# Kernel tuning notes

Hardware: AMD Instinct MI355X
Metric: run time of the kernel (lower is better)

The kernel has to match this reference:

```python
import jax, jax.numpy as jnp
import numpy as np

CAL = {
 'x': (-0.0025095, 0.0022181),
 'onnxMatMul_166': (-0.22075387835502625, 0.208940327167511),
 'fc1MatMul': (-0.00291599917, 0.0017367251),
 'fc1bias': (-0.48688140511512756, 0.5176185369491577),
 'fc1Add': (-0.48778465390205383, 0.5181604027748108),
 'Wiz_1': (-0.43284985423088074, 0.46175122261047363),
 'Wir_1': (-0.34401071071624756, 0.29191476106643677),
 'Win_1': (-0.3236880302429199, 0.39607325196266174),
 'Whz_1': (-1.8417714834213257, 1.7173254489898682),
 'Whr_1': (-1.1574513912200928, 1.0300449132919312),
 'Whn_1': (-0.7756922245025635, 0.9530389308929443),
 'biz_1': (-0.5063393712043762, 0.36664387583732605),
 'bir_1': (-0.07920225709676743, 0.20611026883125305),
 'bin_1': (-0.5539973378181458, 0.17938342690467834),
 'bhz_1': (-0.5337516665458679, 0.4148772358894348),
 'bhr_1': (-0.07688436657190323, 0.14814253151416779),
 'bhn_1': (-0.7828555107116699, 0.9008108973503113),
 'Wiz_2': (-0.9102030992507935, 0.9408696889877319),
 'Wir_2': (-0.9560997486114502, 0.6683358550071716),
 'Win_2': (-0.4721935987472534, 0.48561596870422363),
 'Whz_2': (-1.2992678880691528, 1.2991048097610474),
 'Whr_2': (-0.8318714499473572, 1.1085889339447021),
 'Whn_2': (-0.955470085144043, 1.046797513961792),
 'biz_2': (-0.44805487990379333, 0.1560053527355194),
 'bir_2': (-0.08767592161893845, 0.11347303539514542),
 'bin_2': (-0.239909827709198, 0.12033259868621826),
 'bhz_2': (-0.43745461106300354, 0.12699371576309204),
 'bhr_2': (-0.09617264568805695, 0.07690174877643585),
 'bhn_2': (-0.17204178869724274, 0.19739042222499847),
 'onnxMatMul_207': (-1.3657219409942627, 1.158295750617981),
 'fc2bias': (-0.1750922054052353, 0.1385071724653244),
 'onnxMatMul_208': (-3.1666038036346436, 2.5026357173919678),
 'fc3bias': (-0.10188056528568268, 0.0899151861667633),
 'onnxMatMul_209': (-1.300571084022522, 1.928941249847412),
 'fc4bias': (-0.10699586570262909, 0.04597663879394531),
 'h1': (-0.002647488145157695, 0.0028339680284261703),
 'h2': (-0.0031016061548143625, 0.0030250486452132463),
 'gru1_a_': (-0.6389939785003662, 0.7715625762939453),
 'gru1_a': (-0.6046768426895142, 0.8871182203292847),
 'gru1_b_': (-0.004922409541904926, 0.004103424027562141),
 'gru1_b': (-0.07475128024816513, 0.14630259573459625),
 'gru1_c_': (-1.5660111904144287, 1.0454494953155518),
 'gru1_c': (-1.9779117107391357, 1.3700535297393799),
 'gru1_d_': (-0.008429044857621193, 0.006403823848813772),
 'gru1_d': (-0.5529640316963196, 0.41507571935653687),
 'gru1_e_': (-1.3637111186981201, 1.018247127532959),
 'gru1_e': (-1.8583884239196777, 1.1587692499160767),
 'gru1_f_': (-0.005411399528384209, 0.0061536869034171104),
 'gru1_f': (-0.7833794355392456, 0.8978855013847351),
 'gru1_r_': (-0.6226556301116943, 0.9800534844398499),
 'gru1_r': (0.3491777181625366, 0.7271188497543335),
 'gru1_z_': (-2.392332077026367, 1.7851293087005615),
 'gru1_z': (0.08375928550958633, 0.856329083442688),
 'gru1_n1': (-0.5516456365585327, 0.4556601643562317),
 'gru1_n2': (-2.4100341796875, 1.1423156261444092),
 'gru1_n': (-0.983996570110321, 0.8151924014091492),
 'gru1_hn1': (0.143670916557312, 0.9162406921386719),
 'gru1_hn2': (-0.9015777111053467, 0.45391541719436646),
 'gru1_hn3': (-0.0016954239690676332, 0.0016671211924403906),
 'rnn1GRU': (-0.9016271829605103, 0.4546271562576294),
 'gru2_a_': (-0.681461751461029, 0.9113116264343262),
 'gru2_a': (-0.7149235010147095, 0.908741295337677),
 'gru2_b_': (-0.005148397758603096, 0.011014967225492),
 'gru2_b': (-0.09436552226543427, 0.07623167335987091),
 'gru2_c_': (-1.2279887199401855, 1.1102137565612793),
 'gru2_c': (-1.6760436296463013, 1.200895071029663),
 'gru2_d_': (-0.008141756057739258, 0.00894666276872158),
 'gru2_d': (-0.43875735998153687, 0.1262134611606598),
 'gru2_e_': (-0.6732944250106812, 0.6314664483070374),
}
# calib entries for gru2 past 'e_' were truncated in the source; reuse gru1 ranges
for _k in ['e', 'f_', 'f', 'r_', 'r', 'z_', 'z', 'n1', 'n2', 'n', 'hn1', 'hn2', 'hn3']:
    CAL.setdefault('gru2_' + _k, CAL['gru1_' + _k])
CAL['rnn2GRU'] = CAL['rnn1GRU']


def fq(x, name):
    """Per-tensor unsigned 8-bit fake-quantize/dequantize (CalibrationParam S/Z)."""
    mn, mx = CAL[name]
    s = (mx - mn) / 255.0  # 2**8 - 1
    z = float(round(-mn / s))
    q = jnp.clip(jnp.round(x / s) + z, 0.0, 255.0)
    y = (q - z) * s
    # straight-through: forward value is exact fake-quant, identity gradient
    return x + jax.lax.stop_gradient(y - x)


def _gru_layer(xs, Wiz, Wir, Win, Whz, Whr, Whn, biz, bir, binn, bhz, bhr, bhn, L):
    p = 'gru%d' % L
    Wiz = fq(Wiz, 'Wiz_%d' % L); Wir = fq(Wir, 'Wir_%d' % L); Win = fq(Win, 'Win_%d' % L)
    Whz = fq(Whz, 'Whz_%d' % L); Whr = fq(Whr, 'Whr_%d' % L); Whn = fq(Whn, 'Whn_%d' % L)
    biz = fq(biz, 'biz_%d' % L); bir = fq(bir, 'bir_%d' % L); binn = fq(binn, 'bin_%d' % L)
    bhz = fq(bhz, 'bhz_%d' % L); bhr = fq(bhr, 'bhr_%d' % L); bhn = fq(bhn, 'bhn_%d' % L)
    # input projections batched over all timesteps (xs: [T,B,H] time-major)
    A = fq(fq(jnp.einsum('tbi,ih->tbh', xs, Wir), p + '_a_') + bir, p + '_a')
    C = fq(fq(jnp.einsum('tbi,ih->tbh', xs, Wiz), p + '_c_') + biz, p + '_c')
    E = fq(fq(jnp.einsum('tbi,ih->tbh', xs, Win), p + '_e_') + binn, p + '_e')
    h0 = fq(jnp.zeros((xs.shape[1], Whz.shape[0]), xs.dtype), 'h%d' % L)

    def step(h, ace):
        a, c, e = ace
        b = fq(fq(h @ Whr, p + '_b_') + bhr, p + '_b')
        r = fq(jax.nn.sigmoid(fq(a + b, p + '_r_')), p + '_r')
        d = fq(fq(h @ Whz, p + '_d_') + bhz, p + '_d')
        z = fq(jax.nn.sigmoid(fq(c + d, p + '_z_')), p + '_z')
        f = fq(fq(h @ Whn, p + '_f_') + bhn, p + '_f')
        n = fq(jnp.tanh(fq(e + fq(r * f, p + '_n1'), p + '_n2')), p + '_n')
        hn2 = fq(fq(1.0 - z, p + '_hn1') * n, p + '_hn2')
        hn3 = fq(z * h, p + '_hn3')
        h_new = fq(hn2 + hn3, 'rnn%dGRU' % L)
        return h_new, h_new

    _, hs = jax.lax.scan(step, h0, (A, C, E))
    return hs


def setup_inputs() -> dict:
    B, T, F, H, D = 64, 1000, 257, 400, 600
    ks = iter(jax.random.split(jax.random.key(0), 64))

    def u(shape, name):
        mn, mx = CAL[name]
        return jax.random.uniform(next(ks), shape, jnp.float32, mn, mx)

    inp = {}
    inp['x'] = jax.random.normal(next(ks), (B, T, F), jnp.float32) * 0.001
    inp['W_fc1'] = u((F, H), 'onnxMatMul_166')
    inp['b_fc1'] = u((H,), 'fc1bias')
    for L in (1, 2):
        for g in ('z', 'r', 'n'):
            inp['Wi%s%d' % (g, L)] = u((H, H), 'Wi%s_%d' % (g, L))
            inp['Wh%s%d' % (g, L)] = u((H, H), 'Wh%s_%d' % (g, L))
            inp['bi%s%d' % (g, L)] = u((H,), 'bi%s_%d' % (g, L))
            inp['bh%s%d' % (g, L)] = u((H,), 'bh%s_%d' % (g, L))
    inp['W_fc2'] = u((H, D), 'onnxMatMul_207'); inp['b_fc2'] = u((D,), 'fc2bias')
    inp['W_fc3'] = u((D, D), 'onnxMatMul_208'); inp['b_fc3'] = u((D,), 'fc3bias')
    inp['W_fc4'] = u((D, F), 'onnxMatMul_209'); inp['b_fc4'] = u((F,), 'fc4bias')
    return inp


def reference(x, W_fc1, b_fc1, Wiz1, Wir1, Win1, Whz1, Whr1, Whn1, biz1, bir1, bin1, bhz1, bhr1, bhn1, Wiz2, Wir2, Win2, Whz2, Whr2, Whn2, biz2, bir2, bin2, bhz2, bhr2, bhn2, W_fc2, b_fc2, W_fc3, b_fc3, W_fc4, b_fc4):
    xq = fq(x, 'x')
    t = fq(jnp.einsum('bti,ih->bth', xq, fq(W_fc1, 'onnxMatMul_166')), 'fc1MatMul')
    t = fq(t + fq(b_fc1, 'fc1bias'), 'fc1Add')
    xs = jnp.swapaxes(t, 0, 1)  # [T,B,400]
    h1 = _gru_layer(xs, Wiz1, Wir1, Win1, Whz1, Whr1, Whn1, biz1, bir1, bin1, bhz1, bhr1, bhn1, 1)
    h2 = _gru_layer(h1, Wiz2, Wir2, Win2, Whz2, Whr2, Whn2, biz2, bir2, bin2, bhz2, bhr2, bhn2, 2)
    y = jnp.swapaxes(h2, 0, 1)  # [B,T,400]
    y = jax.nn.relu(jnp.einsum('bth,hd->btd', y, fq(W_fc2, 'onnxMatMul_207')) + fq(b_fc2, 'fc2bias'))
    y = jax.nn.relu(jnp.einsum('btd,de->bte', y, fq(W_fc3, 'onnxMatMul_208')) + fq(b_fc3, 'fc3bias'))
    y = jax.nn.sigmoid(jnp.einsum('bte,ef->btf', y, fq(W_fc4, 'onnxMatMul_209')) + fq(b_fc4, 'fc4bias'))
    return y
```

## Files before the change

### kernel.cpp

```cpp
#include <hip/hip_runtime.h>
#include <math.h>

#define DEV static __device__ __forceinline__

typedef int v4i __attribute__((ext_vector_type(4)));
typedef float v4f __attribute__((ext_vector_type(4)));
typedef __bf16 bf16_t;
typedef __bf16 v8bf __attribute__((ext_vector_type(8)));

struct SZ { float s, z; };

constexpr double cfloor_(double v){ long long i=(long long)v; return ((double)i > v) ? (double)(i-1) : (double)i; }
constexpr double cround_(double v){
  double fl = cfloor_(v); double fr = v - fl;
  return (fr > 0.5) ? fl + 1.0 : (fr < 0.5 ? fl : ((((long long)fl) & 1LL) == 0 ? fl : fl + 1.0));
}
constexpr SZ mksz(double mn, double mx){
  double s = (mx - mn) / 255.0;
  double z = cround_(-mn / s);
  return SZ{ (float)s, (float)z };
}

constexpr SZ Zx     = mksz(-0.0025095, 0.0022181);
constexpr SZ ZW1    = mksz(-0.22075387835502625, 0.208940327167511);
// ... 108 lines not shown
    float q = rintf(jb.W[m][k * 400 + j] / jb.s[m]) + jb.z[m];
    q = fminf(fmaxf(q, 0.f), 255.f);
    dst[i] = (unsigned char)q;
  }
}
__global__ __launch_bounds__(256) void kcolsum(const unsigned char* __restrict__ WhC, int* __restrict__ cs){
  int i = blockIdx.x * 256 + threadIdx.x;
  if (i < 2400) {
    const unsigned char* p = WhC + (size_t)i * 400;
    int s = 0;
    for (int k = 0; k < 400; ++k) s += p[k];
    cs[i] = s;
  }
}
__global__ __launch_bounds__(256) void kwic6(W6 jb, signed char* __restrict__ WiT, int* __restrict__ cs){
  for (int idx = blockIdx.x * 256 + threadIdx.x; idx < 960000; idx += gridDim.x * 256) {
    int m = idx / 160000, r = idx - m * 160000;
    int k = r / 400, n = r - k * 400;
    float q = rintf(jb.W[m][r] / jb.s[m]) + jb.z[m];
    q = fminf(fmaxf(q, 0.f), 255.f);
    int qi = (int)q;
    WiT[(size_t)m * 185600 + (size_t)n * 464 + k] = (signed char)(qi ^ 0x80);
    atomicAdd(&cs[m * 400 + n], qi - 128);
  }
  for (int idx = blockIdx.x * 256 + threadIdx.x; idx < 153600; idx += gridDim.x * 256) {
    int m = idx / 25600, r = idx - m * 25600;
    int n = r / 64, p = r - n * 64;
    WiT[(size_t)m * 185600 + (size_t)n * 464 + 400 + p] = 0;
  }
}
__global__ __launch_bounds__(256) void kwic(const float* __restrict__ W, signed char* __restrict__ Bt,
                                            int* __restrict__ cs, float s, float z, int K, int N){
  int total1 = K * N, total2 = (464 - K) * N;
  for (int idx = blockIdx.x * 256 + threadIdx.x; idx < total1; idx += gridDim.x * 256) {
    int k = idx / N, n = idx - k * N;
    float q = rintf(W[idx] / s) + z;
    q = fminf(fmaxf(q, 0.f), 255.f);
    int qi = (int)q;
    Bt[(size_t)n * 464 + k] = (signed char)(qi ^ 0x80);
    atomicAdd(&cs[n], qi - 128);
  }
  for (int idx = blockIdx.x * 256 + threadIdx.x; idx < total2; idx += gridDim.x * 256) {
    int n = idx / (464 - K), k = K + (idx - n * (464 - K));
    Bt[(size_t)n * 464 + k] = 0;
  }
}
__global__ __launch_bounds__(256) void kwbf(const float* __restrict__ W, bf16_t* __restrict__ Bt,
                                            float s, float z, int K, int N){
  int total1 = K * N, total2 = (608 - K) * N;
  for (int idx = blockIdx.x * 256 + threadIdx.x; idx < total1; idx += gridDim.x * 256) {
    int k = idx / N, n = idx - k * N;
    float q = rintf(W[idx] / s) + z;
    q = fminf(fmaxf(q, 0.f), 255.f);
    Bt[(size_t)n * 608 + k] = (bf16_t)(q - z);
  }
  for (int idx = blockIdx.x * 256 + threadIdx.x; idx < total2; idx += gridDim.x * 256) {
    int n = idx / (608 - K), k = K + (idx - n * (608 - K));
    Bt[(size_t)n * 608 + k] = (bf16_t)0.f;
  }
}
__global__ __launch_bounds__(256) void kxq(const float* __restrict__ x, unsigned char* __restrict__ xcq,
                                           float s, float z){
  int idx = blockIdx.x * 256 + threadIdx.x;
  if (idx < 64000 * 464) {
    int row = idx / 464, c = idx - row * 464;
    unsigned char code = 128;
    if (c < 257) {
      int bb = row & 63, tt = row >> 6;
      float q = rintf(x[((size_t)bb * 1000 + tt) * 257 + c] / s) + z;
      q = fminf(fmaxf(q, 0.f), 255.f);
      code = (unsigned char)q;
    }
    xcq[idx] = code;
  }
}
__global__ __launch_bounds__(256) void krsum(const unsigned char* __restrict__ A, int* __restrict__ rs,
                                             int w4){
  int r = blockIdx.x * 256 + threadIdx.x;
  const unsigned* p = (const unsigned*)(A + (size_t)r * (w4 * 16));
  unsigned s = 0;
  for (int i = 0; i < w4 * 4; ++i) s = udot4_(p[i], 0x01010101u, s);
  rs[r] = (int)s - 128 * 4 * (w4 * 4);
}
__global__ __launch_bounds__(256) void kinit(unsigned long long* __restrict__ hp1,
                                             unsigned long long* __restrict__ hp2, unsigned code){
  int i = blockIdx.x * 256 + threadIdx.x;
  if (i < 6400) {
    unsigned long long w = (unsigned long long)(code * 0x01010101u);
    hp1[i] = w; hp2[i] = w;
  }
}

__global__ __launch_bounds__(256) void gemm_i8(
    const unsigned char* __restrict__ Au8, int strideA, int aw4,
    const int* __restrict__ rowsum,
    const signed char* __restrict__ Bt, const int* __restrict__ colsum,
    const float* __restrict__ bias,
    unsigned char* __restrict__ outU8, float* __restrict__ outF,
    int N, int nb, int outStride, int epMode,
    int czw, int cza, int cconst, float ss,
    float e1S, float e1Z, float e2S, float e2Z)
{
  __shared__ __align__(16) signed char Asl[64 * 464];
  __shared__ __align__(16) signed char Bsl[80 * 464];
  const int tid = threadIdx.x;
  const int bm = blockIdx.x / nb;
  const int bn = blockIdx.x - bm * nb;
  const int m0 = bm * 64;
  const int n0 = bn * 80;
  for (int i = tid; i < 80 * 29; i += 256) {
    int r = i / 29, c = i - r * 29;
    uint4 v;
    if (n0 + r < N) v = *(const uint4*)(Bt + (size_t)(n0 + r) * 464 + c * 16);
    else { v.x = 0u; v.y = 0u; v.z = 0u; v.w = 0u; }
    *(uint4*)(Bsl + (size_t)r * 464 + c * 16) = v;
  }
  for (int i = tid; i < 64 * 29; i += 256) {
    int r = i / 29, c = i - r * 29;
    uint4 v;
    if (c < aw4) {
      v = *(const uint4*)(Au8 + (size_t)(m0 + r) * strideA + c * 16);
      v.x ^= 0x80808080u; v.y ^= 0x80808080u; v.z ^= 0x80808080u; v.w ^= 0x80808080u;
    } else { v.x = 0u; v.y = 0u; v.z = 0u; v.w = 0u; }
    *(uint4*)(Asl + (size_t)r * 464 + c * 16) = v;
  }
  __syncthreads();
  const int wv = tid >> 6, ln = tid & 63;
  const int lr = ln & 15;
  const int lk = ln >> 4;
  v4i acc[5];
#pragma unroll
  for (int j = 0; j < 5; ++j) { acc[j][0] = 0; acc[j][1] = 0; acc[j][2] = 0; acc[j][3] = 0; }
#pragma unroll
  for (int kc = 0; kc < 7; ++kc) {
    int kb = kc * 64 + lk * 16;
    v4i a = *(const v4i*)(Asl + (size_t)(wv * 16 + lr) * 464 + kb);
#pragma unroll
    for (int j = 0; j < 5; ++j) {
      v4i b = *(const v4i*)(Bsl + (size_t)(j * 16 + lr) * 464 + kb);
      acc[j] = __builtin_amdgcn_mfma_i32_16x16x64_i8(a, b, acc[j], 0, 0, 0);
    }
  }
#pragma unroll
  for (int reg = 0; reg < 4; ++reg) {
    int row = m0 + wv * 16 + lk * 4 + reg;
    int RA = rowsum[row];
#pragma unroll
    for (int j = 0; j < 5; ++j) {
      int col = n0 + j * 16 + lr;
      if (col >= N) continue;
      int I = acc[j][reg] + czw * RA + cza * colsum[col] + cconst;
      float v = (float)I * ss;
      if (epMode == 0) {
        v = fq_(v, e1S, e1Z) + bias[col];
        float q = rintf(v / e2S) + e2Z;
        q = fminf(fmaxf(q, 0.f), 255.f);
        outU8[(size_t)row * outStride + col] = (unsigned char)q;
      } else {
        v += bias[col];
        v = fmaxf(v, 0.f);
        outF[(size_t)row * outStride + col] = v;
      }
    }
  }
}

__global__ __launch_bounds__(512) void gemm_bf(
    const float* __restrict__ A, const bf16_t* __restrict__ Bt,
    const float* __restrict__ bias, float* __restrict__ outF,
    int N, int nb, int epMode, int rowOff, float sc)
{
  __shared__ __align__(16) bf16_t Bs[128 * 616];
  const int tid = threadIdx.x;
  const int bm = blockIdx.x / nb;
  const int bn = blockIdx.x - bm * nb;
  const int m0 = bm * 128;
  const int n0 = bn * 128;
  for (int i = tid; i < 128 * 76; i += 512) {
    int r = i / 76, c = i - r * 76;
    uint4 v; v.x = 0u; v.y = 0u; v.z = 0u; v.w = 0u;
    if (n0 + r < N) v = *(const uint4*)((const char*)(Bt + (size_t)(n0 + r) * 608) + c * 16);
    *(uint4*)((char*)(Bs + (size_t)r * 616) + c * 16) = v;
  }
  __syncthreads();
  const int wv = tid >> 6, ln = tid & 63;
  const int lr = ln & 15, quad = ln >> 4;
  const float* arp = A + (size_t)(m0 + wv * 16 + lr) * 600;
  v4f acc[8];
#pragma unroll
  for (int j = 0; j < 8; ++j) { acc[j][0] = 0.f; acc[j][1] = 0.f; acc[j][2] = 0.f; acc[j][3] = 0.f; }
  for (int kc = 0; kc < 19; ++kc) {
    int kb = kc * 32 + quad * 8;
    float af[8];
    if (kc == 18 && quad == 3) {
#pragma unroll
      for (int j = 0; j < 8; ++j) af[j] = 0.f;
    } else {
      *(float4*)&af[0] = *(const float4*)(arp + kb);
      *(float4*)&af[4] = *(const float4*)(arp + kb + 4);
    }
    v8bf ah, al;
#pragma unroll
    for (int j = 0; j < 8; ++j) {
      float xx = af[j];
      bf16_t h = (bf16_t)xx;
      ah[j] = h;
      al[j] = (bf16_t)(xx - (float)h);
    }
#pragma unroll
    for (int nf = 0; nf < 8; ++nf) {
      v8bf bfrag = *(const v8bf*)(Bs + (size_t)(nf * 16 + lr) * 616 + kc * 32 + quad * 8);
      acc[nf] = __builtin_amdgcn_mfma_f32_16x16x32_bf16(ah, bfrag, acc[nf], 0, 0, 0);
      acc[nf] = __builtin_amdgcn_mfma_f32_16x16x32_bf16(al, bfrag, acc[nf], 0, 0, 0);
    }
  }
#pragma unroll
  for (int nf = 0; nf < 8; ++nf) {
    int col = n0 + nf * 16 + lr;
    if (col >= N) continue;
    float bcol = bias[col];
#pragma unroll
    for (int reg = 0; reg < 4; ++reg) {
      int row = m0 + wv * 16 + quad * 4 + reg;
      float v = acc[nf][reg] * sc + bcol;
      if (epMode == 2) {
        v = fmaxf(v, 0.f);
        outF[(size_t)row * N + col] = v;
      } else {
        v = sigm_(v);
        int rg = rowOff + row;
        int tt = rg >> 6, bb = rg & 63;
        outF[((size_t)bb * 1000 + tt) * 257 + col] = v;
      }
    }
  }
}

__global__ __launch_bounds__(384) void gru_rec(
    const unsigned char* __restrict__ WhC, const int* __restrict__ colsum,
    const unsigned char* __restrict__ Aq, const unsigned char* __restrict__ Cq,
    const unsigned char* __restrict__ Eq,
    const float* __restrict__ bhr, const float* __restrict__ bhz, const float* __restrict__ bhn,
    unsigned char* __restrict__ hs,
    unsigned long long* hpub, RecP P)
{
  __shared__ __align__(16) uint4 Wlds[9600];
  __shared__ __align__(16) uint4 hq_own[7];
  __shared__ __align__(16) uint4 hqr[21];
  __shared__ float dots[2][3][100];
  __shared__ unsigned aceb[75];
  __shared__ int HqS_s;
  __shared__ int flag;

  const int tid = threadIdx.x;
  const int wv  = tid >> 6;
  const int ln  = tid & 63;
  const int b   = blockIdx.x & 63;
  const int sl  = blockIdx.x >> 6;
  const int jbase = sl * 100;

  unsigned* Wled = (unsigned*)Wlds;
  unsigned* hqow = (unsigned*)hq_own;
  unsigned* hqrw = (unsigned*)hqr;

  for (int idx = tid; idx < 30000; idx += 384) {
    int cid0 = idx / 100, w = idx - cid0 * 100;
    int c = w / 25, p = w - c * 25;
    int g0 = cid0 / 100, jj0 = cid0 - g0 * 100;
    unsigned word = ((const unsigned*)(WhC + ((size_t)(g0 * 400) + jbase + jj0) * 400))[w];
    int slot = (c * 7 + (p >> 2)) ^ (cid0 & 31);
    Wled[cid0 * 128 + slot * 4 + (p & 3)] = word;
  }
  for (int idx = tid; idx < 3600; idx += 384) {
    int cid0 = idx / 12, r = idx - cid0 * 12;
    int c = r / 3, wd = r - c * 3 + 1;
    int slot = (c * 7 + 6) ^ (cid0 & 31);
    Wled[cid0 * 128 + slot * 4 + wd] = 0u;
  }
  const unsigned code0 = (unsigned)fminf(fmaxf(P.rnn.z, 0.f), 255.f);
  if (tid < 28) hqow[tid] = (tid < 25) ? code0 * 0x01010101u : 0u;
  if (tid >= 32 && tid < 41) {
    int r = tid - 32; int o = r / 3, wd = r - o * 3 + 1;
    hqrw[o * 28 + 24 + wd] = 0u;
  }
  if (tid == 383) flag = -1;

  const int cid = tid;
  int g = cid / 100;
  int jj = cid - g * 100;
  float s1S = 1.f, s1Z = 0.f, s2S = 1.f, s2Z = 0.f, biasj = 0.f, swsh = 0.f;
  int zwi = 0, CSj = 0;
  if (tid < 300) {
    int j = jbase + jj;
    SZ w  = (g == 0) ? P.wr : (g == 1) ? P.wz : P.wn;
    SZ s1 = (g == 0) ? P.b1 : (g == 1) ? P.d1 : P.f1;
    SZ s2 = (g == 0) ? P.b2 : (g == 1) ? P.d2 : P.f2;
    zwi = (int)w.z;
    s1S = s1.s; s1Z = s1.z; s2S = s2.s; s2Z = s2.z;
    biasj = ((g == 0) ? bhr : (g == 1) ? bhz : bhn)[j];
    CSj = colsum[g * 400 + j];
    swsh = w.s * P.rnn.s;
  }
  const int zhi = (int)P.rnn.z;
  const int swm = cid & 31;

  unsigned hprev = code0;
  __syncthreads();

  for (int t = 0; t < 1000; ++t) {
    if (wv == 5) {
      size_t row = (size_t)t * 64 + b;
      int w0 = ln, w1 = 64 + ln;
      int wh0 = w0 / 25, wi0 = w0 - wh0 * 25;
      const unsigned char* p0 = (wh0 == 0) ? Aq : (wh0 == 1) ? Cq : Eq;
      unsigned v0 = *(const unsigned*)(p0 + row * 400 + jbase + wi0 * 4);
      unsigned v1 = 0;
      if (ln < 11) {
        int wh1 = w1 / 25, wi1 = w1 - wh1 * 25;
        const unsigned char* p1 = (wh1 == 0) ? Aq : (wh1 == 1) ? Cq : Eq;
        v1 = *(const unsigned*)(p1 + row * 400 + jbase + wi1 * 4);
      }
      const unsigned long long* base = hpub + ((size_t)(t & 3) * 64 + b) * 100;
      unsigned pay0, pay1 = 0;
      {
        int o = ln / 25, p = ln - o * 25;
        int so = (sl + o + 1) & 3;
        const unsigned long long* src = base + so * 25 + p;
        unsigned long long w64;
        while ((unsigned)((w64 = __hip_atomic_load(src, __ATOMIC_RELAXED, __HIP_MEMORY_SCOPE_AGENT)) >> 32)
               != (unsigned)t) { }
        pay0 = (unsigned)w64;
        hqrw[o * 28 + ((p >> 2) * 4) + (p & 3)] = pay0;
      }
      if (ln < 11) {
        int widx = 64 + ln;
        int o = widx / 25, p = widx - o * 25;
        int so = (sl + o + 1) & 3;
        const unsigned long long* src = base + so * 25 + p;
        unsigned long long w64;
        while ((unsigned)((w64 = __hip_atomic_load(src, __ATOMIC_RELAXED, __HIP_MEMORY_SCOPE_AGENT)) >> 32)
               != (unsigned)t) { }
        pay1 = (unsigned)w64;
        hqrw[o * 28 + ((p >> 2) * 4) + (p & 3)] = pay1;
      }
      unsigned hp = udot4_(pay0, 0x01010101u, 0u);
      if (ln < 11) hp = udot4_(pay1, 0x01010101u, hp);
      if (ln < 25) hp = udot4_(hqow[ln], 0x01010101u, hp);
#pragma unroll
      for (int off = 32; off; off >>= 1) hp += __shfl_down(hp, off, 64);
      if (ln == 0) HqS_s = (int)hp;
      __hip_atomic_store(&flag, t, __ATOMIC_RELEASE, __HIP_MEMORY_SCOPE_WORKGROUP);
      aceb[ln] = v0;
      if (ln < 11) aceb[64 + ln] = v1;
      if (t > 0 && ln < 25)
        *(unsigned*)(hs + ((size_t)(t - 1) * 64 + b) * 400 + jbase + ln * 4) = hqow[ln];
    } else if (tid < 300) {
      unsigned acc = 0;
      const uint4* wcol = &Wlds[cid * 32];
#pragma unroll
      for (int i = 0; i < 7; ++i) {
        uint4 h = hq_own[i];
        uint4 w = wcol[(sl * 7 + i) ^ swm];
        acc = udot4_(w.x, h.x, acc);
        acc = udot4_(w.y, h.y, acc);
        acc = udot4_(w.z, h.z, acc);
        acc = udot4_(w.w, h.w, acc);
      }
      while (__hip_atomic_load(&flag, __ATOMIC_ACQUIRE, __HIP_MEMORY_SCOPE_WORKGROUP) < t)
        __builtin_amdgcn_s_sleep(1);
#pragma unroll
      for (int o = 0; o < 3; ++o) {
        int c = (sl + o + 1) & 3;
#pragma unroll
        for (int i = 0; i < 7; ++i) {
          uint4 h = hqr[o * 7 + i];
          uint4 w = wcol[(c * 7 + i) ^ swm];
          acc = udot4_(w.x, h.x, acc);
          acc = udot4_(w.y, h.y, acc);
          acc = udot4_(w.z, h.z, acc);
          acc = udot4_(w.w, h.w, acc);
        }
      }
      int I = (int)acc - zwi * HqS_s - zhi * CSj + 400 * zhi * zwi;
      float dot = (float)I * swsh;
      float v = fq_(dot, s1S, s1Z) + biasj;
      v = fq_(v, s2S, s2Z);
      dots[t & 1][g][jj] = v;
    }
    __syncthreads();
    if (tid < 128) {
      int m = (tid < 100) ? tid : 99;
      const unsigned char* aceb8 = (const unsigned char*)aceb;
      float a = ((float)aceb8[m]       - P.a.z) * P.a.s;
      float c = ((float)aceb8[100 + m] - P.c.z) * P.c.s;
      float e = ((float)aceb8[200 + m] - P.e.z) * P.e.s;
      float bb = dots[t & 1][0][m], dd = dots[t & 1][1][m], ff = dots[t & 1][2][m];
      float r  = fq_(sigm_(fq_(a + bb, P.r1.s, P.r1.z)), P.r2.s, P.r2.z);
      float zz = fq_(sigm_(fq_(c + dd, P.z1.s, P.z1.z)), P.z2.s, P.z2.z);
      float nn = fq_(tanhf(fq_(e + fq_(r * ff, P.n1.s, P.n1.z), P.n2.s, P.n2.z)), P.n3.s, P.n3.z);
      float hold = ((float)hprev - P.rnn.z) * P.rnn.s;
      float hn2v = fq_(fq_(1.f - zz, P.hn1.s, P.hn1.z) * nn, P.hn2.s, P.hn2.z);
      float hn3v = fq_(zz * hold, P.hn3.s, P.hn3.z);
      float hnew = hn2v + hn3v;
      float q = rintf(hnew / P.rnn.s) + P.rnn.z;
      q = fminf(fmaxf(q, 0.f), 255.f);
      unsigned code = (unsigned)q;
      unsigned c1 = __shfl_down(code, 1);
      unsigned c2 = __shfl_down(code, 2);
      unsigned c3 = __shfl_down(code, 3);
      if (tid < 100) {
        if ((tid & 3) == 0) {
          unsigned packed = code | (c1 << 8) | (c2 << 16) | (c3 << 24);
          unsigned long long out64 = ((unsigned long long)(unsigned)(t + 1) << 32) | packed;
          unsigned long long* dst = hpub + ((size_t)((t + 1) & 3) * 64 + b) * 100 + sl * 25 + (tid >> 2);
          __hip_atomic_store(dst, out64, __ATOMIC_RELAXED, __HIP_MEMORY_SCOPE_AGENT);
          hqow[tid >> 2] = packed;
        }
        hprev = code;
      }
    }
    __syncthreads();
  }
  if (wv == 5 && ln < 25)
    *(unsigned*)(hs + ((size_t)999 * 64 + b) * 400 + jbase + ln * 4) = hqow[ln];
}

extern "C" void kernel_launch(void* const* d_in, const int* in_sizes, int n_in,
                              void* d_out, int out_size, void* d_ws, size_t ws_size,
                              hipStream_t stream)
{
  const float* x    = (const float*)d_in[0];
  const float* Wfc1 = (const float*)d_in[1];
  const float* bfc1 = (const float*)d_in[2];
  const float* Wiz1 = (const float*)d_in[3];  const float* Whz1 = (const float*)d_in[4];
  const float* biz1 = (const float*)d_in[5];  const float* bhz1 = (const float*)d_in[6];
  const float* Wir1 = (const float*)d_in[7];  const float* Whr1 = (const float*)d_in[8];
  const float* bir1 = (const float*)d_in[9];  const float* bhr1 = (const float*)d_in[10];
  const float* Win1 = (const float*)d_in[11]; const float* Whn1 = (const float*)d_in[12];
  const float* bin1 = (const float*)d_in[13]; const float* bhn1 = (const float*)d_in[14];
  const float* Wiz2 = (const float*)d_in[15]; const float* Whz2 = (const float*)d_in[16];
  const float* biz2 = (const float*)d_in[17]; const float* bhz2 = (const float*)d_in[18];
  const float* Wir2 = (const float*)d_in[19]; const float* Whr2 = (const float*)d_in[20];
  const float* bir2 = (const float*)d_in[21]; const float* bhr2 = (const float*)d_in[22];
  const float* Win2 = (const float*)d_in[23]; const float* Whn2 = (const float*)d_in[24];
  const float* bin2 = (const float*)d_in[25]; const float* bhn2 = (const float*)d_in[26];
  const float* Wfc2 = (const float*)d_in[27]; const float* bfc2 = (const float*)d_in[28];
  const float* Wfc3 = (const float*)d_in[29]; const float* bfc3 = (const float*)d_in[30];
  const float* Wfc4 = (const float*)d_in[31]; const float* bfc4 = (const float*)d_in[32];
  float* out = (float*)d_out;

  char* wp = (char*)d_ws;
  auto alloc = [&](size_t bytes) -> void* {
    void* p = (void*)wp;
    wp += (bytes + 255) & ~(size_t)255;
    return p;
  };
  float* b1q = (float*)alloc(400 * 4);
  float* biq = (float*)alloc(2400 * 4);
  float* bhq = (float*)alloc(2400 * 4);
  float* b2q = (float*)alloc(600 * 4);
  float* b3q = (float*)alloc(600 * 4);
  float* b4q = (float*)alloc(257 * 4);
  unsigned char* WhC = (unsigned char*)alloc(960000);
  int* colsum = (int*)alloc(2400 * 4);
  signed char* WiT = (signed char*)alloc(7 * 400 * 464);
  signed char* Bt2 = (signed char*)alloc(600 * 464);
  bf16_t* Bt3 = (bf16_t*)alloc(600 * 608 * 2);
  bf16_t* Bt4 = (bf16_t*)alloc(257 * 608 * 2);
  int* cwi = (int*)alloc((7 * 400 + 600) * 4);
  int* rsX1 = (int*)alloc(64000 * 4);
  int* rsX  = (int*)alloc(64000 * 4);
  int* rsH  = (int*)alloc(64000 * 4);
  int* rsH2 = (int*)alloc(64000 * 4);
  unsigned char* xsq = (unsigned char*)alloc(25600000);
  unsigned char* Aq  = (unsigned char*)alloc(25600000);
  unsigned char* Cq  = (unsigned char*)alloc(25600000);
  unsigned char* Eq  = (unsigned char*)alloc(25600000);
  unsigned char* hs1 = (unsigned char*)alloc(25600000);
  unsigned char* hs2 = (unsigned char*)alloc(25600000);
  unsigned long long* hpub1 = (unsigned long long*)alloc(4 * 64 * 100 * 8);
  unsigned long long* hpub2 = (unsigned long long*)alloc(4 * 64 * 100 * 8);
  float* y2c = (float*)Aq;
  float* y3c = (float*)(Aq + 38400000);
  unsigned char* xcq = hs1;

  BJobs bj;
  bj.j[0]  = { bfc1, b1q,        400, Zbfc1.s, Zbfc1.z };
  bj.j[1]  = { bir1, biq + 0,    400, Zbir1.s, Zbir1.z };
  bj.j[2]  = { biz1, biq + 400,  400, Zbiz1.s, Zbiz1.z };
  bj.j[3]  = { bin1, biq + 800,  400, Zbin1.s, Zbin1.z };
  bj.j[4]  = { bir2, biq + 1200, 400, Zbir2.s, Zbir2.z };
  bj.j[5]  = { biz2, biq + 1600, 400, Zbiz2.s, Zbiz2.z };
  bj.j[6]  = { bin2, biq + 2000, 400, Zbin2.s, Zbin2.z };
  bj.j[7]  = { bhr1, bhq + 0,    400, Zbhr1.s, Zbhr1.z };
  bj.j[8]  = { bhz1, bhq + 400,  400, Zbhz1.s, Zbhz1.z };
  bj.j[9]  = { bhn1, bhq + 800,  400, Zbhn1.s, Zbhn1.z };
  bj.j[10] = { bhr2, bhq + 1200, 400, Zbhr2.s, Zbhr2.z };
  bj.j[11] = { bhz2, bhq + 1600, 400, Zbhz2.s, Zbhz2.z };
  bj.j[12] = { bhn2, bhq + 2000, 400, Zbhn2.s, Zbhn2.z };
  bj.j[13] = { bfc2, b2q,        600, Zbfc2.s, Zbfc2.z };
  bj.j[14] = { bfc3, b3q,        600, Zbfc3.s, Zbfc3.z };
  bj.j[15] = { bfc4, b4q,        257, Zbfc4.s, Zbfc4.z };
  kbias<<<dim3(16), dim3(256), 0, stream>>>(bj);

  W6 wh = { { Whr1, Whz1, Whn1, Whr2, Whz2, Whn2 },
            { ZWhr1.s, ZWhz1.s, ZWhn1.s, ZWhr2.s, ZWhz2.s, ZWhn2.s },
            { ZWhr1.z, ZWhz1.z, ZWhn1.z, ZWhr2.z, ZWhz2.z, ZWhn2.z } };
  kwhc6<<<dim3(3750), dim3(256), 0, stream>>>(wh, WhC);
  kcolsum<<<dim3(10), dim3(256), 0, stream>>>(WhC, colsum);
  unsigned code0 = (unsigned)(Zrnn.z < 0.f ? 0.f : (Zrnn.z > 255.f ? 255.f : Zrnn.z));
  kinit<<<dim3(25), dim3(256), 0, stream>>>(hpub1, hpub2, code0);

  hipMemsetAsync(cwi, 0, (7 * 400 + 600) * 4, stream);
  W6 wi = { { Wir1, Wiz1, Win1, Wir2, Wiz2, Win2 },
            { ZWir1.s, ZWiz1.s, ZWin1.s, ZWir2.s, ZWiz2.s, ZWin2.s },
            { ZWir1.z, ZWiz1.z, ZWin1.z, ZWir2.z, ZWiz2.z, ZWin2.z } };
  kwic6<<<dim3(625), dim3(256), 0, stream>>>(wi, WiT, cwi);
  kwic<<<dim3(625), dim3(256), 0, stream>>>(Wfc1, WiT + (size_t)6 * 185600, cwi + 2400, ZW1.s, ZW1.z, 257, 400);
  kwic<<<dim3(625), dim3(256), 0, stream>>>(Wfc2, Bt2, cwi + 2800, ZWfc2.s, ZWfc2.z, 400, 600);
  kwbf<<<dim3(625), dim3(256), 0, stream>>>(Wfc3, Bt3, ZWfc3.s, ZWfc3.z, 600, 600);
  kwbf<<<dim3(625), dim3(256), 0, stream>>>(Wfc4, Bt4, ZWfc4.s, ZWfc4.z, 600, 257);

  auto gi8 = [&](const unsigned char* A, int strideA, int aw4, const int* rs,
                 const signed char* Bt, const int* cs, const float* bias,
                 unsigned char* oU8, float* oF, int M, int N, int outStride, int epMode,
                 SZ a, SZ w, int Kreal, float ss, SZ e1, SZ e2) {
    int czw = 128 - (int)w.z, cza = 128 - (int)a.z;
    int cconst = Kreal * cza * czw;
    int nb = (N + 79) / 80;
    gemm_i8<<<dim3((M / 64) * nb), dim3(256), 0, stream>>>(
        A, strideA, aw4, rs, Bt, cs, bias, oU8, oF, N, nb, outStride, epMode,
        czw, cza, cconst, ss, e1.s, e1.z, e2.s, e2.z);
  };

  kxq<<<dim3((64000 * 464 + 255) / 256), dim3(256), 0, stream>>>(x, xcq, Zx.s, Zx.z);
  krsum<<<dim3(250), dim3(256), 0, stream>>>(xcq, rsX1, 29);
  gi8(xcq, 464, 29, rsX1, WiT + (size_t)6 * 185600, cwi + 2400, b1q,
      xsq, nullptr, 64000, 400, 400, 0, Zx, ZW1, 257, Zx.s * ZW1.s, Zfc1mm, Zfc1add);

  krsum<<<dim3(250), dim3(256), 0, stream>>>(xsq, rsX, 25);
  gi8(xsq, 400, 25, rsX, WiT + (size_t)0 * 185600, cwi + 0,    biq + 0,   Aq, nullptr,
      64000, 400, 400, 0, Zfc1add, ZWir1, 400, Zfc1add.s * ZWir1.s, Za_1, Za1);
  gi8(xsq, 400, 25, rsX, WiT + (size_t)1 * 185600, cwi + 400,  biq + 400, Cq, nullptr,
      64000, 400, 400, 0, Zfc1add, ZWiz1, 400, Zfc1add.s * ZWiz1.s, Zc_1, Zc1);
  gi8(xsq, 400, 25, rsX, WiT + (size_t)2 * 185600, cwi + 800,  biq + 800, Eq, nullptr,
      64000, 400, 400, 0, Zfc1add, ZWin1, 400, Zfc1add.s * ZWin1.s, Ze_1, Ze1);
  gru_rec<<<dim3(256), dim3(384), 0, stream>>>(WhC, colsum, Aq, Cq, Eq,
                                               bhq + 0, bhq + 400, bhq + 800,
                                               hs1, hpub1, PL1);
  krsum<<<dim3(250), dim3(256), 0, stream>>>(hs1, rsH, 25);
  gi8(hs1, 400, 25, rsH, WiT + (size_t)3 * 185600, cwi + 1200, biq + 1200, Aq, nullptr,
      64000, 400, 400, 0, Zrnn, ZWir2, 400, Zrnn.s * ZWir2.s, Za_2, Za2);
  gi8(hs1, 400, 25, rsH, WiT + (size_t)4 * 185600, cwi + 1600, biq + 1600, Cq, nullptr,
      64000, 400, 400, 0, Zrnn, ZWiz2, 400, Zrnn.s * ZWiz2.s, Zc_2, Zc2);
  gi8(hs1, 400, 25, rsH, WiT + (size_t)5 * 185600, cwi + 2000, biq + 2000, Eq, nullptr,
      64000, 400, 400, 0, Zrnn, ZWin2, 400, Zrnn.s * ZWin2.s, Ze_2, Ze1);
  gru_rec<<<dim3(256), dim3(384), 0, stream>>>(WhC + 480000, colsum + 1200, Aq, Cq, Eq,
                                               bhq + 1200, bhq + 1600, bhq + 2000,
                                               hs2, hpub2, PL2);
  krsum<<<dim3(250), dim3(256), 0, stream>>>(hs2, rsH2, 25);
  for (int rc = 0; rc < 4; ++rc) {
    const unsigned char* a2 = hs2 + (size_t)rc * 16000 * 400;
    gi8(a2, 400, 25, rsH2 + rc * 16000, Bt2, cwi + 2800, b2q, nullptr, y2c,
        16000, 600, 600, 2, Zrnn, ZWfc2, 400, Zrnn.s * ZWfc2.s, Zrnn, Zrnn);
    gemm_bf<<<dim3(125 * 5), dim3(512), 0, stream>>>(y2c, Bt3, b3q, y3c, 600, 5, 2, 0, ZWfc3.s);
    gemm_bf<<<dim3(125 * 3), dim3(512), 0, stream>>>(y3c, Bt4, b4q, out, 257, 3, 3, rc * 16000, ZWfc4.s);
  }
  (void)in_sizes; (void)n_in; (void)out_size; (void)ws_size;
}
```

Before: 7.347 ms.

## Run each GRU batch row in a single 768-thread block without cross-block flags

Measured after the change: 13.37 ms. 1.82x slower.

```diff
diff --git a/kernel.cpp b/kernel.cpp
--- a/kernel.cpp
+++ b/kernel.cpp
@@ -214,14 +214,6 @@
   for (int i = 0; i < w4 * 4; ++i) s = udot4_(p[i], 0x01010101u, s);
   rs[r] = (int)s - 128 * 4 * (w4 * 4);
 }
-__global__ __launch_bounds__(256) void kinit(unsigned long long* __restrict__ hp1,
-                                             unsigned long long* __restrict__ hp2, unsigned code){
-  int i = blockIdx.x * 256 + threadIdx.x;
-  if (i < 6400) {
-    unsigned long long w = (unsigned long long)(code * 0x01010101u);
-    hp1[i] = w; hp2[i] = w;
-  }
-}
 
 __global__ __launch_bounds__(256) void gemm_i8(
     const unsigned char* __restrict__ Au8, int strideA, int aw4,
@@ -368,193 +360,190 @@
   }
 }
 
-__global__ __launch_bounds__(384) void gru_rec(
+__global__ __launch_bounds__(768) void gru_rec64(
     const unsigned char* __restrict__ WhC, const int* __restrict__ colsum,
     const unsigned char* __restrict__ Aq, const unsigned char* __restrict__ Cq,
     const unsigned char* __restrict__ Eq,
     const float* __restrict__ bhr, const float* __restrict__ bhz, const float* __restrict__ bhn,
-    unsigned char* __restrict__ hs,
-    unsigned long long* hpub, RecP P)
+    unsigned char* __restrict__ hs, RecP P)
 {
-  __shared__ __align__(16) uint4 Wlds[9600];
-  __shared__ __align__(16) uint4 hq_own[7];
-  __shared__ __align__(16) uint4 hqr[21];
-  __shared__ float dots[2][3][100];
-  __shared__ unsigned aceb[75];
-  __shared__ int HqS_s;
-  __shared__ int flag;
+  __shared__ __align__(16) unsigned Wl[960 * 28];
+  __shared__ __align__(16) unsigned hq[2][4 * 28];
+  __shared__ int dots_i[1200];
+  __shared__ unsigned acew[2][300];
+  __shared__ int ic_l[1200];
+  __shared__ float bias_l[1200];
+  __shared__ int HqS[2];
 
   const int tid = threadIdx.x;
-  const int wv  = tid >> 6;
-  const int ln  = tid & 63;
-  const int b   = blockIdx.x & 63;
-  const int sl  = blockIdx.x >> 6;
-  const int jbase = sl * 100;
-
-  unsigned* Wled = (unsigned*)Wlds;
-  unsigned* hqow = (unsigned*)hq_own;
-  unsigned* hqrw = (unsigned*)hqr;
-
-  for (int idx = tid; idx < 30000; idx += 384) {
-    int cid0 = idx / 100, w = idx - cid0 * 100;
-    int c = w / 25, p = w - c * 25;
-    int g0 = cid0 / 100, jj0 = cid0 - g0 * 100;
-    unsigned word = ((const unsigned*)(WhC + ((size_t)(g0 * 400) + jbase + jj0) * 400))[w];
-    int slot = (c * 7 + (p >> 2)) ^ (cid0 & 31);
-    Wled[cid0 * 128 + slot * 4 + (p & 3)] = word;
-  }
-  for (int idx = tid; idx < 3600; idx += 384) {
-    int cid0 = idx / 12, r = idx - cid0 * 12;
-    int c = r / 3, wd = r - c * 3 + 1;
-    int slot = (c * 7 + 6) ^ (cid0 & 31);
-    Wled[cid0 * 128 + slot * 4 + wd] = 0u;
+  const int b = blockIdx.x;
+  const unsigned* Wu = (const unsigned*)WhC;
+
+  unsigned wq[5][25];
+#pragma unroll
+  for (int s = 0; s < 5; ++s) {
+    int q = tid + 768 * s;
+    const unsigned* src = Wu + (q >> 2) * 100 + (q & 3) * 25;
+#pragma unroll
+    for (int w = 0; w < 25; ++w) wq[s][w] = src[w];
+  }
+  for (int i = tid; i < 960 * 25; i += 768) {
+    int ql = i / 25, w = i - ql * 25;
+    int q = 3840 + ql;
+    Wl[ql * 28 + w] = Wu[(q >> 2) * 100 + (q & 3) * 25 + w];
+  }
+  const int zh = (int)P.rnn.z;
+  for (int d = tid; d < 1200; d += 768) {
+    int g = (d >= 800) ? 2 : (d >= 400 ? 1 : 0);
+    int zw = (g == 0) ? (int)P.wr.z : (g == 1) ? (int)P.wz.z : (int)P.wn.z;
+    ic_l[d] = -zh * colsum[d] + 400 * zh * zw;
+    int j = d - g * 400;
+    bias_l[d] = ((g == 0) ? bhr : (g == 1) ? bhz : bhn)[j];
   }
   const unsigned code0 = (unsigned)fminf(fmaxf(P.rnn.z, 0.f), 255.f);
-  if (tid < 28) hqow[tid] = (tid < 25) ? code0 * 0x01010101u : 0u;
-  if (tid >= 32 && tid < 41) {
-    int r = tid - 32; int o = r / 3, wd = r - o * 3 + 1;
-    hqrw[o * 28 + 24 + wd] = 0u;
-  }
-  if (tid == 383) flag = -1;
-
-  const int cid = tid;
-  int g = cid / 100;
-  int jj = cid - g * 100;
-  float s1S = 1.f, s1Z = 0.f, s2S = 1.f, s2Z = 0.f, biasj = 0.f, swsh = 0.f;
-  int zwi = 0, CSj = 0;
-  if (tid < 300) {
-    int j = jbase + jj;
-    SZ w  = (g == 0) ? P.wr : (g == 1) ? P.wz : P.wn;
-    SZ s1 = (g == 0) ? P.b1 : (g == 1) ? P.d1 : P.f1;
-    SZ s2 = (g == 0) ? P.b2 : (g == 1) ? P.d2 : P.f2;
-    zwi = (int)w.z;
-    s1S = s1.s; s1Z = s1.z; s2S = s2.s; s2Z = s2.z;
-    biasj = ((g == 0) ? bhr : (g == 1) ? bhz : bhn)[j];
-    CSj = colsum[g * 400 + j];
-    swsh = w.s * P.rnn.s;
-  }
-  const int zhi = (int)P.rnn.z;
-  const int swm = cid & 31;
-
-  unsigned hprev = code0;
+  for (int i = tid; i < 100; i += 768)
+    hq[0][(i / 25) * 28 + (i % 25)] = code0 * 0x01010101u;
+  if (tid == 0) { HqS[0] = 400 * (int)code0; HqS[1] = 0; }
+  const unsigned char* psrc = nullptr;
+  int poff = 0;
+  if (tid >= 400 && tid < 700) {
+    int idx = tid - 400;
+    int g = idx / 100, w = idx - g * 100;
+    psrc = (g == 0) ? Aq : (g == 1) ? Cq : Eq;
+    poff = w * 4;
+    acew[0][idx] = *(const unsigned*)(psrc + (size_t)b * 400 + poff);
+  }
   __syncthreads();
 
+  const int part = tid & 3;
+  const int grp = tid >> 2;
+  const unsigned* hbase0 = &hq[0][part * 28];
+  const unsigned* hbase1 = &hq[1][part * 28];
+  const unsigned* wl5 = &Wl[tid * 28];
+  const unsigned* wl6 = &Wl[(768 + (tid & 191)) * 28];
+  const int zwr = (int)P.wr.z, zwz = (int)P.wz.z, zwn = (int)P.wn.z;
+  const float swr = P.wr.s * P.rnn.s, swz = P.wz.s * P.rnn.s, swn = P.wn.s * P.rnn.s;
+
+  unsigned pf = 0;
+  unsigned hcode = code0;
+
   for (int t = 0; t < 1000; ++t) {
-    if (wv == 5) {
-      size_t row = (size_t)t * 64 + b;
-      int w0 = ln, w1 = 64 + ln;
-      int wh0 = w0 / 25, wi0 = w0 - wh0 * 25;
-      const unsigned char* p0 = (wh0 == 0) ? Aq : (wh0 == 1) ? Cq : Eq;
-      unsigned v0 = *(const unsigned*)(p0 + row * 400 + jbase + wi0 * 4);
-      unsigned v1 = 0;
-      if (ln < 11) {
-        int wh1 = w1 / 25, wi1 = w1 - wh1 * 25;
-        const unsigned char* p1 = (wh1 == 0) ? Aq : (wh1 == 1) ? Cq : Eq;
-        v1 = *(const unsigned*)(p1 + row * 400 + jbase + wi1 * 4);
+    if (tid >= 400 && tid < 700) {
+      int tn = (t + 1 < 1000) ? (t + 1) : 999;
+      pf = *(const unsigned*)(psrc + ((size_t)tn * 64 + b) * 400 + poff);
+    }
+    if (tid == 767) HqS[(t + 1) & 1] = 0;
+    const unsigned* hb = (t & 1) ? hbase1 : hbase0;
+    unsigned a0 = 0, a1 = 0, a2 = 0, a3 = 0, a4 = 0, a5 = 0, a6 = 0;
+#pragma unroll
+    for (int c = 0; c < 6; ++c) {
+      uint4 h4 = *(const uint4*)(hb + 4 * c);
+      uint4 w5 = *(const uint4*)(wl5 + 4 * c);
+      a0 = udot4_(wq[0][4*c+0], h4.x, a0);
+      a0 = udot4_(wq[0][4*c+1], h4.y, a0);
+      a0 = udot4_(wq[0][4*c+2], h4.z, a0);
+      a0 = udot4_(wq[0][4*c+3], h4.w, a0);
+      a1 = udot4_(wq[1][4*c+0], h4.x, a1);
+      a1 = udot4_(wq[1][4*c+1], h4.y, a1);
+      a1 = udot4_(wq[1][4*c+2], h4.z, a1);
+      a1 = udot4_(wq[1][4*c+3], h4.w, a1);
+      a2 = udot4_(wq[2][4*c+0], h4.x, a2);
+      a2 = udot4_(wq[2][4*c+1], h4.y, a2);
+      a2 = udot4_(wq[2][4*c+2], h4.z, a2);
+      a2 = udot4_(wq[2][4*c+3], h4.w, a2);
+      a3 = udot4_(wq[3][4*c+0], h4.x, a3);
+      a3 = udot4_(wq[3][4*c+1], h4.y, a3);
+      a3 = udot4_(wq[3][4*c+2], h4.z, a3);
+      a3 = udot4_(wq[3][4*c+3], h4.w, a3);
+      a4 = udot4_(wq[4][4*c+0], h4.x, a4);
+      a4 = udot4_(wq[4][4*c+1], h4.y, a4);
+      a4 = udot4_(wq[4][4*c+2], h4.z, a4);
+      a4 = udot4_(wq[4][4*c+3], h4.w, a4);
+      a5 = udot4_(w5.x, h4.x, a5);
+      a5 = udot4_(w5.y, h4.y, a5);
+      a5 = udot4_(w5.z, h4.z, a5);
+      a5 = udot4_(w5.w, h4.w, a5);
+      if (tid < 192) {
+        uint4 w6 = *(const uint4*)(wl6 + 4 * c);
+        a6 = udot4_(w6.x, h4.x, a6);
+        a6 = udot4_(w6.y, h4.y, a6);
+        a6 = udot4_(w6.z, h4.z, a6);
+        a6 = udot4_(w6.w, h4.w, a6);
       }
-      const unsigned long long* base = hpub + ((size_t)(t & 3) * 64 + b) * 100;
-      unsigned pay0, pay1 = 0;
-      {
-        int o = ln / 25, p = ln - o * 25;
-        int so = (sl + o + 1) & 3;
-        const unsigned long long* src = base + so * 25 + p;
-        unsigned long long w64;
-        while ((unsigned)((w64 = __hip_atomic_load(src, __ATOMIC_RELAXED, __HIP_MEMORY_SCOPE_AGENT)) >> 32)
-               != (unsigned)t) { }
-        pay0 = (unsigned)w64;
-        hqrw[o * 28 + ((p >> 2) * 4) + (p & 3)] = pay0;
-      }
-      if (ln < 11) {
-        int widx = 64 + ln;
-        int o = widx / 25, p = widx - o * 25;
-        int so = (sl + o + 1) & 3;
-        const unsigned long long* src = base + so * 25 + p;
-        unsigned long long w64;
-        while ((unsigned)((w64 = __hip_atomic_load(src, __ATOMIC_RELAXED, __HIP_MEMORY_SCOPE_AGENT)) >> 32)
-               != (unsigned)t) { }
-        pay1 = (unsigned)w64;
-        hqrw[o * 28 + ((p >> 2) * 4) + (p & 3)] = pay1;
-      }
-      unsigned hp = udot4_(pay0, 0x01010101u, 0u);
-      if (ln < 11) hp = udot4_(pay1, 0x01010101u, hp);
-      if (ln < 25) hp = udot4_(hqow[ln], 0x01010101u, hp);
-#pragma unroll
-      for (int off = 32; off; off >>= 1) hp += __shfl_down(hp, off, 64);
-      if (ln == 0) HqS_s = (int)hp;
-      __hip_atomic_store(&flag, t, __ATOMIC_RELEASE, __HIP_MEMORY_SCOPE_WORKGROUP);
-      aceb[ln] = v0;
-      if (ln < 11) aceb[64 + ln] = v1;
-      if (t > 0 && ln < 25)
-        *(unsigned*)(hs + ((size_t)(t - 1) * 64 + b) * 400 + jbase + ln * 4) = hqow[ln];
-    } else if (tid < 300) {
-      unsigned acc = 0;
-      const uint4* wcol = &Wlds[cid * 32];
-#pragma unroll
-      for (int i = 0; i < 7; ++i) {
-        uint4 h = hq_own[i];
-        uint4 w = wcol[(sl * 7 + i) ^ swm];
-        acc = udot4_(w.x, h.x, acc);
-        acc = udot4_(w.y, h.y, acc);
-        acc = udot4_(w.z, h.z, acc);
-        acc = udot4_(w.w, h.w, acc);
-      }
-      while (__hip_atomic_load(&flag, __ATOMIC_ACQUIRE, __HIP_MEMORY_SCOPE_WORKGROUP) < t)
-        __builtin_amdgcn_s_sleep(1);
-#pragma unroll
-      for (int o = 0; o < 3; ++o) {
-        int c = (sl + o + 1) & 3;
-#pragma unroll
-        for (int i = 0; i < 7; ++i) {
-          uint4 h = hqr[o * 7 + i];
-          uint4 w = wcol[(c * 7 + i) ^ swm];
-          acc = udot4_(w.x, h.x, acc);
-          acc = udot4_(w.y, h.y, acc);
-          acc = udot4_(w.z, h.z, acc);
-          acc = udot4_(w.w, h.w, acc);
-        }
-      }
-      int I = (int)acc - zwi * HqS_s - zhi * CSj + 400 * zhi * zwi;
-      float dot = (float)I * swsh;
-      float v = fq_(dot, s1S, s1Z) + biasj;
-      v = fq_(v, s2S, s2Z);
-      dots[t & 1][g][jj] = v;
+    }
+    {
+      unsigned hl = hb[24];
+      a0 = udot4_(wq[0][24], hl, a0);
+      a1 = udot4_(wq[1][24], hl, a1);
+      a2 = udot4_(wq[2][24], hl, a2);
+      a3 = udot4_(wq[3][24], hl, a3);
+      a4 = udot4_(wq[4][24], hl, a4);
+      a5 = udot4_(wl5[24], hl, a5);
+      if (tid < 192) a6 = udot4_(wl6[24], hl, a6);
+    }
+    a0 += __shfl_xor(a0, 1); a0 += __shfl_xor(a0, 2);
+    a1 += __shfl_xor(a1, 1); a1 += __shfl_xor(a1, 2);
+    a2 += __shfl_xor(a2, 1); a2 += __shfl_xor(a2, 2);
+    a3 += __shfl_xor(a3, 1); a3 += __shfl_xor(a3, 2);
+    a4 += __shfl_xor(a4, 1); a4 += __shfl_xor(a4, 2);
+    a5 += __shfl_xor(a5, 1); a5 += __shfl_xor(a5, 2);
+    a6 += __shfl_xor(a6, 1); a6 += __shfl_xor(a6, 2);
+    {
+      int v0 = (part == 0) ? (int)a0 : (part == 1) ? (int)a1 : (part == 2) ? (int)a2 : (int)a3;
+      dots_i[grp + 192 * part] = v0;
+      if (part == 0)      dots_i[grp + 768]  = (int)a4;
+      else if (part == 1) dots_i[grp + 960]  = (int)a5;
+      else if (part == 2) { if (grp < 48) dots_i[grp + 1152] = (int)a6; }
     }
     __syncthreads();
-    if (tid < 128) {
-      int m = (tid < 100) ? tid : 99;
-      const unsigned char* aceb8 = (const unsigned char*)aceb;
-      float a = ((float)aceb8[m]       - P.a.z) * P.a.s;
-      float c = ((float)aceb8[100 + m] - P.c.z) * P.c.s;
-      float e = ((float)aceb8[200 + m] - P.e.z) * P.e.s;
-      float bb = dots[t & 1][0][m], dd = dots[t & 1][1][m], ff = dots[t & 1][2][m];
-      float r  = fq_(sigm_(fq_(a + bb, P.r1.s, P.r1.z)), P.r2.s, P.r2.z);
-      float zz = fq_(sigm_(fq_(c + dd, P.z1.s, P.z1.z)), P.z2.s, P.z2.z);
-      float nn = fq_(tanhf(fq_(e + fq_(r * ff, P.n1.s, P.n1.z), P.n2.s, P.n2.z)), P.n3.s, P.n3.z);
-      float hold = ((float)hprev - P.rnn.z) * P.rnn.s;
+
+    unsigned ps = 0;
+    if (tid < 400) {
+      const int j = tid;
+      const unsigned char* ab = (const unsigned char*)&acew[t & 1][0];
+      float av = ((float)ab[j]       - P.a.z) * P.a.s;
+      float cv = ((float)ab[400 + j] - P.c.z) * P.c.s;
+      float ev = ((float)ab[800 + j] - P.e.z) * P.e.s;
+      int hqs = HqS[t & 1];
+      int Ib = dots_i[j]       - zwr * hqs + ic_l[j];
+      int Id = dots_i[400 + j] - zwz * hqs + ic_l[400 + j];
+      int If = dots_i[800 + j] - zwn * hqs + ic_l[800 + j];
+      float bb = fq_((float)Ib * swr, P.b1.s, P.b1.z) + bias_l[j];
+      bb = fq_(bb, P.b2.s, P.b2.z);
+      float dd = fq_((float)Id * swz, P.d1.s, P.d1.z) + bias_l[400 + j];
+      dd = fq_(dd, P.d2.s, P.d2.z);
+      float ff = fq_((float)If * swn, P.f1.s, P.f1.z) + bias_l[800 + j];
+      ff = fq_(ff, P.f2.s, P.f2.z);
+      float r  = fq_(sigm_(fq_(av + bb, P.r1.s, P.r1.z)), P.r2.s, P.r2.z);
+      float zz = fq_(sigm_(fq_(cv + dd, P.z1.s, P.z1.z)), P.z2.s, P.z2.z);
+      float nn = fq_(tanhf(fq_(ev + fq_(r * ff, P.n1.s, P.n1.z), P.n2.s, P.n2.z)), P.n3.s, P.n3.z);
+      float hold = ((float)hcode - P.rnn.z) * P.rnn.s;
       float hn2v = fq_(fq_(1.f - zz, P.hn1.s, P.hn1.z) * nn, P.hn2.s, P.hn2.z);
       float hn3v = fq_(zz * hold, P.hn3.s, P.hn3.z);
       float hnew = hn2v + hn3v;
-      float q = rintf(hnew / P.rnn.s) + P.rnn.z;
-      q = fminf(fmaxf(q, 0.f), 255.f);
-      unsigned code = (unsigned)q;
+      float qv = rintf(hnew / P.rnn.s) + P.rnn.z;
+      qv = fminf(fmaxf(qv, 0.f), 255.f);
+      unsigned code = (unsigned)qv;
+      hcode = code;
       unsigned c1 = __shfl_down(code, 1);
       unsigned c2 = __shfl_down(code, 2);
       unsigned c3 = __shfl_down(code, 3);
-      if (tid < 100) {
-        if ((tid & 3) == 0) {
-          unsigned packed = code | (c1 << 8) | (c2 << 16) | (c3 << 24);
-          unsigned long long out64 = ((unsigned long long)(unsigned)(t + 1) << 32) | packed;
-          unsigned long long* dst = hpub + ((size_t)((t + 1) & 3) * 64 + b) * 100 + sl * 25 + (tid >> 2);
-          __hip_atomic_store(dst, out64, __ATOMIC_RELAXED, __HIP_MEMORY_SCOPE_AGENT);
-          hqow[tid >> 2] = packed;
-        }
-        hprev = code;
+      if ((j & 3) == 0) {
+        unsigned packed = code | (c1 << 8) | (c2 << 16) | (c3 << 24);
+        int wrd = j >> 2;
+        int pp = wrd / 25, off = wrd - pp * 25;
+        hq[(t + 1) & 1][pp * 28 + off] = packed;
+        *(unsigned*)(hs + ((size_t)t * 64 + b) * 400 + (wrd << 2)) = packed;
+        ps = udot4_(packed, 0x01010101u, 0u);
       }
-    }
+    } else if (tid < 700) {
+      acew[(t + 1) & 1][tid - 400] = pf;
+    }
+#pragma unroll
+    for (int off = 32; off; off >>= 1) ps += __shfl_down(ps, off);
+    if ((tid & 63) == 0) atomicAdd(&HqS[(t + 1) & 1], (int)ps);
     __syncthreads();
   }
-  if (wv == 5 && ln < 25)
-    *(unsigned*)(hs + ((size_t)999 * 64 + b) * 400 + jbase + ln * 4) = hqow[ln];
 }
 
 extern "C" void kernel_launch(void* const* d_in, const int* in_sizes, int n_in,
@@ -610,8 +599,6 @@
   unsigned char* Eq  = (unsigned char*)alloc(25600000);
   unsigned char* hs1 = (unsigned char*)alloc(25600000);
   unsigned char* hs2 = (unsigned char*)alloc(25600000);
-  unsigned long long* hpub1 = (unsigned long long*)alloc(4 * 64 * 100 * 8);
-  unsigned long long* hpub2 = (unsigned long long*)alloc(4 * 64 * 100 * 8);
   float* y2c = (float*)Aq;
   float* y3c = (float*)(Aq + 38400000);
   unsigned char* xcq = hs1;
@@ -640,8 +627,6 @@
             { ZWhr1.z, ZWhz1.z, ZWhn1.z, ZWhr2.z, ZWhz2.z, ZWhn2.z } };
   kwhc6<<<dim3(3750), dim3(256), 0, stream>>>(wh, WhC);
   kcolsum<<<dim3(10), dim3(256), 0, stream>>>(WhC, colsum);
-  unsigned code0 = (unsigned)(Zrnn.z < 0.f ? 0.f : (Zrnn.z > 255.f ? 255.f : Zrnn.z));
-  kinit<<<dim3(25), dim3(256), 0, stream>>>(hpub1, hpub2, code0);
 
   hipMemsetAsync(cwi, 0, (7 * 400 + 600) * 4, stream);
   W6 wi = { { Wir1, Wiz1, Win1, Wir2, Wiz2, Win2 },
@@ -677,9 +662,9 @@
       64000, 400, 400, 0, Zfc1add, ZWiz1, 400, Zfc1add.s * ZWiz1.s, Zc_1, Zc1);
   gi8(xsq, 400, 25, rsX, WiT + (size_t)2 * 185600, cwi + 800,  biq + 800, Eq, nullptr,
       64000, 400, 400, 0, Zfc1add, ZWin1, 400, Zfc1add.s * ZWin1.s, Ze_1, Ze1);
-  gru_rec<<<dim3(256), dim3(384), 0, stream>>>(WhC, colsum, Aq, Cq, Eq,
-                                               bhq + 0, bhq + 400, bhq + 800,
-                                               hs1, hpub1, PL1);
+  gru_rec64<<<dim3(64), dim3(768), 0, stream>>>(WhC, colsum, Aq, Cq, Eq,
+                                                bhq + 0, bhq + 400, bhq + 800,
+                                                hs1, PL1);
   krsum<<<dim3(250), dim3(256), 0, stream>>>(hs1, rsH, 25);
   gi8(hs1, 400, 25, rsH, WiT + (size_t)3 * 185600, cwi + 1200, biq + 1200, Aq, nullptr,
       64000, 400, 400, 0, Zrnn, ZWir2, 400, Zrnn.s * ZWir2.s, Za_2, Za2);
@@ -687,9 +672,9 @@
       64000, 400, 400, 0, Zrnn, ZWiz2, 400, Zrnn.s * ZWiz2.s, Zc_2, Zc2);
   gi8(hs1, 400, 25, rsH, WiT + (size_t)5 * 185600, cwi + 2000, biq + 2000, Eq, nullptr,
       64000, 400, 400, 0, Zrnn, ZWin2, 400, Zrnn.s * ZWin2.s, Ze_2, Ze1);
-  gru_rec<<<dim3(256), dim3(384), 0, stream>>>(WhC + 480000, colsum + 1200, Aq, Cq, Eq,
-                                               bhq + 1200, bhq + 1600, bhq + 2000,
-                                               hs2, hpub2, PL2);
+  gru_rec64<<<dim3(64), dim3(768), 0, stream>>>(WhC + 480000, colsum + 1200, Aq, Cq, Eq,
+                                                bhq + 1200, bhq + 1600, bhq + 2000,
+                                                hs2, PL2);
   krsum<<<dim3(250), dim3(256), 0, stream>>>(hs2, rsH2, 25);
   for (int rc = 0; rc < 4; ++rc) {
     const unsigned char* a2 = hs2 + (size_t)rc * 16000 * 400;
```
